# Kernel optimization log

Measured on AMD Instinct MI355X. Metric: run time of the kernel, lower is better.

The kernel has to match this reference:

```python
import jax, jax.numpy as jnp
import numpy as np

B, S, D_MODEL = 2, 1024, 768
NUM_HEADS = 12
HEAD_DIM = D_MODEL // NUM_HEADS  # 64
W_ONE_SIDED = 32  # attention_window = 64 total (symmetric band of 2w+1 = 65)
OUT_DIM = 768


def setup_inputs() -> dict:
    key = jax.random.key(0)
    ks = jax.random.split(key, 6)
    s = 0.02
    return {
        "layer_embeddings": jax.random.normal(ks[0], (B, S, D_MODEL), jnp.float32),
        "Wq": jax.random.normal(ks[1], (D_MODEL, D_MODEL), jnp.float32) * s,
        "bq": jnp.zeros((D_MODEL,), jnp.float32),
        "Wk": jax.random.normal(ks[2], (D_MODEL, D_MODEL), jnp.float32) * s,
        "bk": jnp.zeros((D_MODEL,), jnp.float32),
        "Wv": jax.random.normal(ks[3], (D_MODEL, D_MODEL), jnp.float32) * s,
        "bv": jnp.zeros((D_MODEL,), jnp.float32),
        "Wfc": jax.random.normal(ks[4], (D_MODEL, OUT_DIM), jnp.float32) * s,
        "bfc": jnp.zeros((OUT_DIM,), jnp.float32),
    }


def reference(layer_embeddings, Wq, bq, Wk, bk, Wv, bv, Wfc, bfc):
    x = layer_embeddings                          # [B, S, D]
    b, s_len, d = x.shape
    q = (x @ Wq + bq).reshape(b, s_len, NUM_HEADS, HEAD_DIM)
    k = (x @ Wk + bk).reshape(b, s_len, NUM_HEADS, HEAD_DIM)
    v = (x @ Wv + bv).reshape(b, s_len, NUM_HEADS, HEAD_DIM)

    w = W_ONE_SIDED
    offs = jnp.arange(-w, w + 1)                  # [band]
    pos = jnp.arange(s_len)[:, None] + offs[None, :]  # [S, band]
    valid = (pos >= 0) & (pos < s_len)
    idx = jnp.clip(pos, 0, s_len - 1)

    # Gather only the banded keys/values (honors the sliding-window sparsity)
    kb = k[:, idx]                                # [B, S, band, H, Dh]
    vb = v[:, idx]                                # [B, S, band, H, Dh]

    scale = 1.0 / np.sqrt(HEAD_DIM).astype(np.float32)
    scores = jnp.einsum('bshd,bswhd->bhsw', q, kb) * scale  # [B, H, S, band]
    scores = jnp.where(valid[None, None, :, :], scores, jnp.float32(-1e9))
    attn = jax.nn.softmax(scores, axis=-1)

    out = jnp.einsum('bhsw,bswhd->bshd', attn, vb).reshape(b, s_len, d)
    pooled = out.mean(axis=1)                     # [B, D]
    return jax.nn.relu(pooled @ Wfc + bfc)        # [B, OUT_DIM]
```

## Files before the change

kernel.cpp:

```cpp
#include <hip/hip_runtime.h>
#include <hip/hip_bf16.h>
#include <stdint.h>

#define S_LEN 1024
#define BATCH 2
#define DM    768
#define NH    12
#define HD    64
#define W1    32
#define WIN   65
#define NQKV  2304
#define M_TOT 2048

typedef unsigned short u16;
typedef __attribute__((ext_vector_type(4))) float f4;
typedef __attribute__((ext_vector_type(4))) unsigned short us4;
typedef __attribute__((ext_vector_type(8))) unsigned short ushort8;
typedef __attribute__((ext_vector_type(8))) __bf16 bf16x8;
typedef __attribute__((ext_vector_type(4))) float f32x4;

__device__ inline float bf2f(u16 x) {
    union { unsigned u; float f; } z;
    z.u = ((unsigned)x) << 16;
    return z.f;
}
__device__ inline u16 f2bf(float x) {
    union { float f; unsigned u; } z;
    z.f = x;
    unsigned r = z.u + 0x7FFF + ((z.u >> 16) & 1);
    return (u16)(r >> 16);
}

__global__ __launch_bounds__(256) void prep(
    const float* __restrict__ X,
    const float* __restrict__ Wq, const float* __restrict__ Wk,
    const float* __restrict__ Wv,
    u16* __restrict__ Xb, u16* __restrict__ Wt,
    float* __restrict__ pooled) {
    __shared__ float tile[64][69];
    const int t = threadIdx.x;
    const int bid = blockIdx.x;

    if (bid < 768) {
        if (bid == 0) {
            #pragma unroll
            for (int i = 0; i < 6; ++i) pooled[i * 256 + t] = 0.f;
        }
        const long base = (long)bid * 2048 + t * 8;
        f4 a = *(const f4*)&X[base];
        f4 b = *(const f4*)&X[base + 4];
        float v[8] = {a.x, a.y, a.z, a.w, b.x, b.y, b.z, b.w};
        ushort8 h;
        #pragma unroll
        for (int j = 0; j < 8; ++j) h[j] = f2bf(v[j]);
        *(ushort8*)&Xb[base] = h;
    } else {
        const int tw = bid - 768;
        const int n0 = (tw % 36) * 64;
        const int k0 = (tw / 36) * 64;
        const int sel = n0 / DM;
        const int nl0 = n0 % DM;
        const float* W = (sel == 0) ? Wq : ((sel == 1) ? Wk : Wv);
        const int r = t >> 3;
        const int cg = t & 7;

        #pragma unroll
        for (int p = 0; p < 2; ++p) {
            int rr = r + p * 32;
            long gb = (long)(k0 + rr) * DM + nl0 + cg * 8;
            *(f4*)&tile[rr][cg * 8]     = *(const f4*)&W[gb];
            *(f4*)&tile[rr][cg * 8 + 4] = *(const f4*)&W[gb + 4];
        }
        __syncthreads();
        #pragma unroll
        for (int p = 0; p < 2; ++p) {
            int rn = r + p * 32;
            ushort8 h;
            #pragma unroll
            for (int jj = 0; jj < 8; ++jj)
                h[jj] = f2bf(tile[cg * 8 + jj][rn]);
            *(ushort8*)&Wt[(long)(n0 + rn) * DM + k0 + cg * 8] = h;
        }
    }
}

__global__ __launch_bounds__(256) void qkv_gemm_mfma(
    const u16* __restrict__ Xb, const u16* __restrict__ Wt,
    const float* __restrict__ bq, const float* __restrict__ bk,
    const float* __restrict__ bv,
    u16* __restrict__ Q, u16* __restrict__ K, u16* __restrict__ Vt) {
    __shared__ u16 As[128 * 64];
    __shared__ u16 Bs[64 * 64];

    const int bid = blockIdx.x;
    const int xcd = bid & 7;
    const int local = bid >> 3;
    const int mt = (xcd & 1) * 8 + (local & 7);
    const int nt = (xcd >> 1) * 9 + (local >> 3);
    const int m0 = mt * 128;
    const int n0 = nt * 64;
    const int t = threadIdx.x;
    const int lane = t & 63;
    const int w = t >> 6;
    const int wm = w * 32;
    const int lrow = lane & 15;
    const int lq = lane >> 4;

    const f32x4 fzero = {0.f, 0.f, 0.f, 0.f};
    f32x4 acc[2][4];
    #pragma unroll
    for (int i = 0; i < 2; ++i)
        #pragma unroll
        for (int j = 0; j < 4; ++j) acc[i][j] = fzero;

    for (int kk = 0; kk < DM; kk += 64) {
        __syncthreads();
        #pragma unroll
        for (int p = 0; p < 4; ++p) {
            int slot = p * 256 + t;
            int row = slot >> 3;
            int skc = slot & 7;
            int sw = skc ^ (row & 7);
            long ga = (long)(m0 + row) * DM + kk + skc * 8;
            *(ushort8*)&As[(row * 8 + sw) * 8] = *(const ushort8*)&Xb[ga];
        }
        #pragma unroll
        for (int p = 0; p < 2; ++p) {
            int slot = p * 256 + t;
            int row = slot >> 3;
            int skc = slot & 7;
            int sw = skc ^ (row & 7);
            long gb = (long)(n0 + row) * DM + kk + skc * 8;
            *(ushort8*)&Bs[(row * 8 + sw) * 8] = *(const ushort8*)&Wt[gb];
        }
        __syncthreads();
        #pragma unroll
        for (int kh = 0; kh < 2; ++kh) {
            const int c = kh * 4 + lq;
            bf16x8 ah[2], bh[4];
            #pragma unroll
            for (int i = 0; i < 2; ++i) {
                int ar = wm + i * 16 + lrow;
                ah[i] = *(const bf16x8*)&As[(ar * 8 + (c ^ (ar & 7))) * 8];
            }
            #pragma unroll
            for (int j = 0; j < 4; ++j) {
                int br = j * 16 + lrow;
                bh[j] = *(const bf16x8*)&Bs[(br * 8 + (c ^ (br & 7))) * 8];
            }
            #pragma unroll
            for (int i = 0; i < 2; ++i)
                #pragma unroll
                for (int j = 0; j < 4; ++j)
                    acc[i][j] = __builtin_amdgcn_mfma_f32_16x16x32_bf16(
                        ah[i], bh[j], acc[i][j], 0, 0, 0);
        }
    }

    const int region = n0 / DM;
    const int nc0 = n0 % DM;
    const float* bias = (region == 0) ? bq : ((region == 1) ? bk : bv);

    if (region < 2) {
        u16* Out = (region == 0) ? Q : K;
        #pragma unroll
        for (int j = 0; j < 4; ++j) {
            int col = nc0 + j * 16 + lrow;
            float bval = bias[col];
            #pragma unroll
            for (int i = 0; i < 2; ++i) {
                int row = m0 + wm + i * 16 + lq * 4;
                #pragma unroll
                for (int r = 0; r < 4; ++r)
                    Out[(long)(row + r) * DM + col] = f2bf(acc[i][j][r] + bval);
            }
        }
    } else {
        const int h = nc0 >> 6;
        #pragma unroll
        for (int j = 0; j < 4; ++j) {
            int dloc = j * 16 + lrow;
            float bval = bias[nc0 + dloc];
            #pragma unroll
            for (int i = 0; i < 2; ++i) {
                int row = m0 + wm + i * 16 + lq * 4;
                int b = row >> 10, sl = row & 1023;
                us4 pk;
                #pragma unroll
                for (int r = 0; r < 4; ++r) pk[r] = f2bf(acc[i][j][r] + bval);
                *(us4*)&Vt[(((long)(b * NH + h) * 64 + dloc) << 10) + sl] = pk;
            }
        }
    }
}

__global__ __launch_bounds__(128) void attn_pool_mfma(
    const u16* __restrict__ Q, const u16* __restrict__ K,
    const u16* __restrict__ Vt, float* __restrict__ pooled) {
    __shared__ u16 vt[64][104];
    __shared__ u16 pl[2][16][104];
    const int b = blockIdx.z, h = blockIdx.y;
    const int s0 = blockIdx.x * 32;
    const int t = threadIdx.x;
    const int k0 = s0 - 32;

    const u16* vtg = Vt + ((size_t)(b * NH + h) * 64) * 1024;
    #pragma unroll
    for (int it = 0; it < 6; ++it) {
        int slot = it * 128 + t;
        int d = slot / 12, kc = slot % 12;
        int kbase = k0 + kc * 8;
        if (kbase >= 0 && kbase + 7 < S_LEN) {
            *(ushort8*)&vt[d][kc * 8] = *(const ushort8*)&vtg[d * 1024 + kbase];
        } else {
            #pragma unroll
            for (int j = 0; j < 8; ++j) {
                int kk = kbase + j;
                int kcl = kk < 0 ? 0 : (kk > S_LEN - 1 ? S_LEN - 1 : kk);
                vt[d][kc * 8 + j] = vtg[d * 1024 + kcl];
            }
        }
    }
    __syncthreads();

    const int w = t >> 6, lane = t & 63;
    const int cl = lane & 15, q = lane >> 4;

    const f32x4 fzero = {0.f, 0.f, 0.f, 0.f};
    f32x4 accS[6];
    #pragma unroll
    for (int n = 0; n < 6; ++n) accS[n] = fzero;

    const long qrow = (long)(b * S_LEN + s0 + w * 16 + cl);
    bf16x8 aq[2];
    #pragma unroll
    for (int ks = 0; ks < 2; ++ks)
        aq[ks] = *(const bf16x8*)&Q[qrow * DM + h * HD + ks * 32 + q * 8];
    #pragma unroll
    for (int n = 0; n < 6; ++n) {
        int key = k0 + n * 16 + cl;
        int kcl = key < 0 ? 0 : (key > S_LEN - 1 ? S_LEN - 1 : key);
        long ka = (long)(b * S_LEN + kcl) * DM + h * HD;
        #pragma unroll
        for (int ks = 0; ks < 2; ++ks) {
            bf16x8 bk = *(const bf16x8*)&K[ka + ks * 32 + q * 8];
            accS[n] = __builtin_amdgcn_mfma_f32_16x16x32_bf16(aq[ks], bk, accS[n], 0, 0, 0);
        }
    }

    float l4[4] = {0.f, 0.f, 0.f, 0.f};
    #pragma unroll
    for (int n = 0; n < 6; ++n) {
        int key = k0 + n * 16 + cl;
        #pragma unroll
        for (int r = 0; r < 4; ++r) {
            int s = s0 + w * 16 + q * 4 + r;
            bool valid = (key >= s - W1) && (key <= s + W1) && (key >= 0) && (key < S_LEN);
            float p = valid ? __expf(accS[n][r] * 0.125f) : 0.f;
            accS[n][r] = p;
            l4[r] += p;
        }
    }
    #pragma unroll
    for (int m = 1; m <= 8; m <<= 1)
        #pragma unroll
        for (int r = 0; r < 4; ++r) l4[r] += __shfl_xor(l4[r], m, 64);

    #pragma unroll
    for (int n = 0; n < 6; ++n)
        #pragma unroll
        for (int r = 0; r < 4; ++r)
            pl[w][q * 4 + r][n * 16 + cl] = f2bf(accS[n][r]);

    f32x4 accO[4];
    #pragma unroll
    for (int n = 0; n < 4; ++n) accO[n] = fzero;
    bf16x8 ap[3];
    #pragma unroll
    for (int ks = 0; ks < 3; ++ks)
        ap[ks] = *(const bf16x8*)&pl[w][cl][ks * 32 + q * 8];
    #pragma unroll
    for (int n = 0; n < 4; ++n)
        #pragma unroll
        for (int ks = 0; ks < 3; ++ks) {
            bf16x8 bv = *(const bf16x8*)&vt[n * 16 + cl][ks * 32 + q * 8];
            accO[n] = __builtin_amdgcn_mfma_f32_16x16x32_bf16(ap[ks], bv, accO[n], 0, 0, 0);
        }

    float rcp4[4];
    #pragma unroll
    for (int r = 0; r < 4; ++r) rcp4[r] = 1.0f / l4[r];
    #pragma unroll
    for (int n = 0; n < 4; ++n) {
        float pp = 0.f;
        #pragma unroll
        for (int r = 0; r < 4; ++r) pp += accO[n][r] * rcp4[r];
        pp += __shfl_xor(pp, 16, 64);
        pp += __shfl_xor(pp, 32, 64);
        if (q == 0)
            atomicAdd(&pooled[b * DM + h * HD + n * 16 + cl], pp);
    }
}

__global__ __launch_bounds__(256) void fc_relu_f(
    const float* __restrict__ pooled, const float* __restrict__ Wfc,
    const float* __restrict__ bfc, float* __restrict__ out) {
    __shared__ float red[4][64];
    const int t = threadIdx.x;
    const int nb = blockIdx.x % 12;
    const int bb = blockIdx.x / 12;
    const int nn = t & 63;
    const int dg = t >> 6;
    const int n = nb * 64 + nn;
    float s = 0.f;
    for (int d = dg * 192; d < dg * 192 + 192; ++d)
        s += pooled[bb * DM + d] * Wfc[(long)d * DM + n];
    red[dg][nn] = s;
    __syncthreads();
    if (t < 64) {
        float sum = red[0][t] + red[1][t] + red[2][t] + red[3][t];
        sum = sum * (1.0f / (float)S_LEN) + bfc[nb * 64 + t];
        sum = sum > 0.f ? sum : 0.f;
        out[bb * DM + nb * 64 + t] = sum;
    }
}

extern "C" void kernel_launch(void* const* d_in, const int* in_sizes, int n_in,
                              void* d_out, int out_size, void* d_ws, size_t ws_size,
                              hipStream_t stream) {
    const float* X   = (const float*)d_in[0];
    const float* Wq  = (const float*)d_in[1];
    const float* bq  = (const float*)d_in[2];
    const float* Wk  = (const float*)d_in[3];
    const float* bk  = (const float*)d_in[4];
    const float* Wv  = (const float*)d_in[5];
    const float* bv  = (const float*)d_in[6];
    const float* Wfc = (const float*)d_in[7];
    const float* bfc = (const float*)d_in[8];

    char* ws = (char*)d_ws;
    const size_t SZ_XB = (size_t)M_TOT * DM * 2;
    const size_t SZ_WB = (size_t)NQKV * DM * 2;
    u16* Xb = (u16*)(ws);
    u16* Wt = (u16*)(ws + SZ_XB);
    u16* Q  = (u16*)(ws + SZ_XB + SZ_WB);
    u16* K  = (u16*)(ws + 2 * SZ_XB + SZ_WB);
    u16* Vt = (u16*)(ws + 3 * SZ_XB + SZ_WB);
    float* pooled = (float*)(ws + 4 * SZ_XB + SZ_WB);

    prep<<<1200, 256, 0, stream>>>(X, Wq, Wk, Wv, Xb, Wt, pooled);

    qkv_gemm_mfma<<<576, 256, 0, stream>>>(
        Xb, Wt, bq, bk, bv, Q, K, Vt);

    attn_pool_mfma<<<dim3(32, NH, BATCH), 128, 0, stream>>>(
        Q, K, Vt, pooled);

    fc_relu_f<<<24, 256, 0, stream>>>(pooled, Wfc, bfc, (float*)d_out);
}
```

Measured before the change: 118.8 us.

## Double-buffer QKV GEMM with direct global-to-LDS loads; replace pooling atomics with partials

The QKV GEMM now uses two LDS buffers filled through global_load_lds, so the next K-tile is fetched while MFMAs run on the current one, and one barrier per step is dropped. The attention kernel writes per-block pooled partials instead of issuing float atomics, and the FC kernel reduces those partials itself, which also removes the zeroing of pooled in prep. The cost is twice the LDS in the GEMM and an extra partial-reduction pass in every FC block. The async LDS writes also depend on the hardware writing lanes contiguously, matching the swizzle computed into the global addresses.

```diff
diff --git a/kernel.cpp b/kernel.cpp
--- a/kernel.cpp
+++ b/kernel.cpp
@@ -31,21 +31,22 @@
     return (u16)(r >> 16);
 }
 
+__device__ __forceinline__ void g2l16(const u16* g, u16* l) {
+    __builtin_amdgcn_global_load_lds(
+        (const __attribute__((address_space(1))) unsigned int*)g,
+        (__attribute__((address_space(3))) unsigned int*)l, 16, 0, 0);
+}
+
 __global__ __launch_bounds__(256) void prep(
     const float* __restrict__ X,
     const float* __restrict__ Wq, const float* __restrict__ Wk,
     const float* __restrict__ Wv,
-    u16* __restrict__ Xb, u16* __restrict__ Wt,
-    float* __restrict__ pooled) {
+    u16* __restrict__ Xb, u16* __restrict__ Wt) {
     __shared__ float tile[64][69];
     const int t = threadIdx.x;
     const int bid = blockIdx.x;
 
     if (bid < 768) {
-        if (bid == 0) {
-            #pragma unroll
-            for (int i = 0; i < 6; ++i) pooled[i * 256 + t] = 0.f;
-        }
         const long base = (long)bid * 2048 + t * 8;
         f4 a = *(const f4*)&X[base];
         f4 b = *(const f4*)&X[base + 4];
@@ -89,8 +90,8 @@
     const float* __restrict__ bq, const float* __restrict__ bk,
     const float* __restrict__ bv,
     u16* __restrict__ Q, u16* __restrict__ K, u16* __restrict__ Vt) {
-    __shared__ u16 As[128 * 64];
-    __shared__ u16 Bs[64 * 64];
+    __shared__ u16 As[2][128 * 64];
+    __shared__ u16 Bs[2][64 * 64];
 
     const int bid = blockIdx.x;
     const int xcd = bid & 7;
@@ -106,6 +107,37 @@
     const int lrow = lane & 15;
     const int lq = lane >> 4;
 
+    const u16* gA[4];
+    const u16* gB[2];
+    #pragma unroll
+    for (int p = 0; p < 4; ++p) {
+        int slot = p * 256 + t;
+        int row = slot >> 3;
+        int skc = (slot & 7) ^ (row & 7);
+        gA[p] = Xb + (long)(m0 + row) * DM + skc * 8;
+    }
+    #pragma unroll
+    for (int p = 0; p < 2; ++p) {
+        int slot = p * 256 + t;
+        int row = slot >> 3;
+        int skc = (slot & 7) ^ (row & 7);
+        gB[p] = Wt + (long)(n0 + row) * DM + skc * 8;
+    }
+
+#define STAGE(buf)                                                          \
+    do {                                                                    \
+        _Pragma("unroll")                                                   \
+        for (int p = 0; p < 4; ++p)                                         \
+            g2l16(gA[p], &As[buf][(p * 256 + w * 64) * 8]);                 \
+        _Pragma("unroll")                                                   \
+        for (int p = 0; p < 2; ++p)                                         \
+            g2l16(gB[p], &Bs[buf][(p * 256 + w * 64) * 8]);                 \
+        _Pragma("unroll")                                                   \
+        for (int p = 0; p < 4; ++p) gA[p] += 64;                            \
+        _Pragma("unroll")                                                   \
+        for (int p = 0; p < 2; ++p) gB[p] += 64;                            \
+    } while (0)
+
     const f32x4 fzero = {0.f, 0.f, 0.f, 0.f};
     f32x4 acc[2][4];
     #pragma unroll
@@ -113,27 +145,13 @@
         #pragma unroll
         for (int j = 0; j < 4; ++j) acc[i][j] = fzero;
 
-    for (int kk = 0; kk < DM; kk += 64) {
-        __syncthreads();
-        #pragma unroll
-        for (int p = 0; p < 4; ++p) {
-            int slot = p * 256 + t;
-            int row = slot >> 3;
-            int skc = slot & 7;
-            int sw = skc ^ (row & 7);
-            long ga = (long)(m0 + row) * DM + kk + skc * 8;
-            *(ushort8*)&As[(row * 8 + sw) * 8] = *(const ushort8*)&Xb[ga];
-        }
-        #pragma unroll
-        for (int p = 0; p < 2; ++p) {
-            int slot = p * 256 + t;
-            int row = slot >> 3;
-            int skc = slot & 7;
-            int sw = skc ^ (row & 7);
-            long gb = (long)(n0 + row) * DM + kk + skc * 8;
-            *(ushort8*)&Bs[(row * 8 + sw) * 8] = *(const ushort8*)&Wt[gb];
-        }
-        __syncthreads();
+    STAGE(0);
+    __syncthreads();
+
+    #pragma unroll
+    for (int ks = 0; ks < 12; ++ks) {
+        const int cb = ks & 1;
+        if (ks < 11) STAGE(cb ^ 1);
         #pragma unroll
         for (int kh = 0; kh < 2; ++kh) {
             const int c = kh * 4 + lq;
@@ -141,12 +159,12 @@
             #pragma unroll
             for (int i = 0; i < 2; ++i) {
                 int ar = wm + i * 16 + lrow;
-                ah[i] = *(const bf16x8*)&As[(ar * 8 + (c ^ (ar & 7))) * 8];
+                ah[i] = *(const bf16x8*)&As[cb][(ar * 8 + (c ^ (ar & 7))) * 8];
             }
             #pragma unroll
             for (int j = 0; j < 4; ++j) {
                 int br = j * 16 + lrow;
-                bh[j] = *(const bf16x8*)&Bs[(br * 8 + (c ^ (br & 7))) * 8];
+                bh[j] = *(const bf16x8*)&Bs[cb][(br * 8 + (c ^ (br & 7))) * 8];
             }
             #pragma unroll
             for (int i = 0; i < 2; ++i)
@@ -155,7 +173,9 @@
                     acc[i][j] = __builtin_amdgcn_mfma_f32_16x16x32_bf16(
                         ah[i], bh[j], acc[i][j], 0, 0, 0);
         }
-    }
+        if (ks < 11) __syncthreads();
+    }
+#undef STAGE
 
     const int region = n0 / DM;
     const int nc0 = n0 % DM;
@@ -196,9 +216,10 @@
 
 __global__ __launch_bounds__(128) void attn_pool_mfma(
     const u16* __restrict__ Q, const u16* __restrict__ K,
-    const u16* __restrict__ Vt, float* __restrict__ pooled) {
+    const u16* __restrict__ Vt, float* __restrict__ partial) {
     __shared__ u16 vt[64][104];
     __shared__ u16 pl[2][16][104];
+    __shared__ float pr[2][64];
     const int b = blockIdx.z, h = blockIdx.y;
     const int s0 = blockIdx.x * 32;
     const int t = threadIdx.x;
@@ -297,24 +318,39 @@
         for (int r = 0; r < 4; ++r) pp += accO[n][r] * rcp4[r];
         pp += __shfl_xor(pp, 16, 64);
         pp += __shfl_xor(pp, 32, 64);
-        if (q == 0)
-            atomicAdd(&pooled[b * DM + h * HD + n * 16 + cl], pp);
+        if (q == 0) pr[w][n * 16 + cl] = pp;
+    }
+    __syncthreads();
+    if (t < 64) {
+        long pb = (((long)(b * NH + h) * 32) + blockIdx.x) * 64 + t;
+        partial[pb] = pr[0][t] + pr[1][t];
     }
 }
 
 __global__ __launch_bounds__(256) void fc_relu_f(
-    const float* __restrict__ pooled, const float* __restrict__ Wfc,
+    const float* __restrict__ partial, const float* __restrict__ Wfc,
     const float* __restrict__ bfc, float* __restrict__ out) {
     __shared__ float red[4][64];
+    __shared__ float ps[768];
     const int t = threadIdx.x;
     const int nb = blockIdx.x % 12;
     const int bb = blockIdx.x / 12;
+
+    for (int d = t; d < DM; d += 256) {
+        const float* pp = partial + ((long)(bb * NH + (d >> 6)) * 32) * 64 + (d & 63);
+        float s = 0.f;
+        #pragma unroll
+        for (int sb = 0; sb < 32; ++sb) s += pp[sb * 64];
+        ps[d] = s;
+    }
+    __syncthreads();
+
     const int nn = t & 63;
     const int dg = t >> 6;
     const int n = nb * 64 + nn;
     float s = 0.f;
     for (int d = dg * 192; d < dg * 192 + 192; ++d)
-        s += pooled[bb * DM + d] * Wfc[(long)d * DM + n];
+        s += ps[d] * Wfc[(long)d * DM + n];
     red[dg][nn] = s;
     __syncthreads();
     if (t < 64) {
@@ -346,15 +382,15 @@
     u16* Q  = (u16*)(ws + SZ_XB + SZ_WB);
     u16* K  = (u16*)(ws + 2 * SZ_XB + SZ_WB);
     u16* Vt = (u16*)(ws + 3 * SZ_XB + SZ_WB);
-    float* pooled = (float*)(ws + 4 * SZ_XB + SZ_WB);
-
-    prep<<<1200, 256, 0, stream>>>(X, Wq, Wk, Wv, Xb, Wt, pooled);
+    float* partial = (float*)(ws + 4 * SZ_XB + SZ_WB);
+
+    prep<<<1200, 256, 0, stream>>>(X, Wq, Wk, Wv, Xb, Wt);
 
     qkv_gemm_mfma<<<576, 256, 0, stream>>>(
         Xb, Wt, bq, bk, bv, Q, K, Vt);
 
     attn_pool_mfma<<<dim3(32, NH, BATCH), 128, 0, stream>>>(
-        Q, K, Vt, pooled);
-
-    fc_relu_f<<<24, 256, 0, stream>>>(pooled, Wfc, bfc, (float*)d_out);
-}
+        Q, K, Vt, partial);
+
+    fc_relu_f<<<24, 256, 0, stream>>>(partial, Wfc, bfc, (float*)d_out);
+}
```

New measurement: 119.1 us. No clear change (+0.3%).
